# Performance work log

Hardware: AMD Instinct MI355X
Metric: run time of the kernel (lower is better)

## Reference

```python
import jax, jax.numpy as jnp
import numpy as np

SCALE = 1.0
STEPS = 5
ALIGN_CORNERS = True
SHAPE = (2, 3, 128, 128, 128)  # N, C(=3 vector comps), D, H, W


def _identity_grid(spatial, align_corners):
    # spatial = (D, H, W); returns [D, H, W, 3] with coords ordered (x, y, z) in [-1, 1],
    # matching torch.nn.functional.grid_sample's grid convention.
    axes = []
    for s in spatial:
        if align_corners:
            axes.append(jnp.linspace(-1.0, 1.0, s, dtype=jnp.float32))
        else:
            axes.append(((2.0 * jnp.arange(s, dtype=jnp.float32) + 1.0) / s) - 1.0)
    zz, yy, xx = jnp.meshgrid(axes[0], axes[1], axes[2], indexing="ij")  # each [D,H,W]
    return jnp.stack([xx, yy, zz], axis=-1)


def _grid_sample_3d(u, grid, align_corners):
    # u: [N, D, H, W, C] channels-last values; grid: [N, D, H, W, 3] (x, y, z) in [-1, 1].
    # Trilinear interpolation with border padding (deepali expv default: PaddingMode.BORDER).
    N, D, H, W, C = u.shape

    def unnorm(g, size):
        if align_corners:
            return (g + 1.0) * 0.5 * (size - 1)
        return ((g + 1.0) * size - 1.0) * 0.5

    x = jnp.clip(unnorm(grid[..., 0], W), 0.0, W - 1)
    y = jnp.clip(unnorm(grid[..., 1], H), 0.0, H - 1)
    z = jnp.clip(unnorm(grid[..., 2], D), 0.0, D - 1)

    x0f, y0f, z0f = jnp.floor(x), jnp.floor(y), jnp.floor(z)
    wx = (x - x0f)[..., None]  # [N,D,H,W,1]
    wy = (y - y0f)[..., None]
    wz = (z - z0f)[..., None]

    x0 = x0f.astype(jnp.int32); x1 = jnp.minimum(x0 + 1, W - 1)
    y0 = y0f.astype(jnp.int32); y1 = jnp.minimum(y0 + 1, H - 1)
    z0 = z0f.astype(jnp.int32); z1 = jnp.minimum(z0 + 1, D - 1)

    b = jnp.arange(N)[:, None, None, None]  # broadcast batch index [N,1,1,1]

    def gather(zi, yi, xi):
        return u[b, zi, yi, xi]  # [N,D,H,W,C]

    # interpolate along x, then y, then z
    c00 = gather(z0, y0, x0) * (1 - wx) + gather(z0, y0, x1) * wx
    c01 = gather(z0, y1, x0) * (1 - wx) + gather(z0, y1, x1) * wx
    c10 = gather(z1, y0, x0) * (1 - wx) + gather(z1, y0, x1) * wx
    c11 = gather(z1, y1, x0) * (1 - wx) + gather(z1, y1, x1) * wx
    c0 = c00 * (1 - wy) + c01 * wy
    c1 = c10 * (1 - wy) + c11 * wy
    return c0 * (1 - wz) + c1 * wz


def setup_inputs() -> dict:
    key = jax.random.key(0)
    # velocity field: small displacements in normalized cube coordinates
    x = jax.random.normal(key, SHAPE, dtype=jnp.float32) * 0.1
    return {"x": x}


def reference(x) -> jnp.ndarray:
    # expv: scaling-and-squaring exponentiation of velocity field x -> displacement field.
    # u <- scale * x / 2^steps; repeat steps times: u <- u + u o u  (self-composition via warp)
    scale = SCALE / (2 ** STEPS)
    u = jnp.moveaxis(x, 1, -1) * scale  # [N, D, H, W, 3], channels (x, y, z)
    grid0 = _identity_grid(x.shape[2:], ALIGN_CORNERS)  # [D, H, W, 3]
    for _ in range(STEPS):
        u = u + _grid_sample_3d(u, grid0[None] + u, ALIGN_CORNERS)
    return jnp.moveaxis(u, -1, 1)  # back to [N, 3, D, H, W]
```

## Files before the change

kernel.cpp:

```cpp
#include <hip/hip_runtime.h>


namespace {
constexpr int kD = 128, kH = 128, kW = 128, kN = 2, kC = 3;
constexpr int kPlane = kD * kH * kW;
constexpr int kVol   = kC * kPlane;
constexpr int kTotalVox   = kN * kPlane;
constexpr int kTotalElems = kN * kVol;
constexpr size_t kBatchBytes = (size_t)kPlane * 6;
constexpr float kScale0 = 1.0f / 32.0f;
}

typedef float f32x2 __attribute__((ext_vector_type(2)));
typedef unsigned int u32;
typedef u32 u32x3 __attribute__((ext_vector_type(3), aligned(4)));
typedef u32 u32x4a4 __attribute__((ext_vector_type(4), aligned(4)));

static __device__ __forceinline__ float h2f(u32 bits) {
    _Float16 v;
    unsigned short s = (unsigned short)bits;
    __builtin_memcpy(&v, &s, 2);
    return (float)v;
}
static __device__ __forceinline__ u32 f2h2(float a, float b) {
    _Float16 ha = (_Float16)a, hb = (_Float16)b;
    unsigned short sa, sb;
    __builtin_memcpy(&sa, &ha, 2);
    __builtin_memcpy(&sb, &hb, 2);
    return (u32)sa | ((u32)sb << 16);
}

static __device__ __forceinline__ int slab_rr(int* n_out, bool rev) {
    int b    = blockIdx.x;
    int xcd  = b & 7;
    int seq  = b >> 3;
    if (rev) seq = 255 - seq;
    int slab = xcd | (((seq >> 7) & 1) << 3);
    *n_out   = slab >> 3;
    int dblk = slab & 7;
    int s7   = seq & 127;
    int ht   = s7 & 31;
    int dt   = (s7 >> 5) & 3;
    int wl   = threadIdx.x & 63;
    int hh   = (threadIdx.x >> 6) & 3;
    int dd   = (threadIdx.x >> 8) & 3;
    int d    = (dblk << 4) | (dt << 2) | dd;
    int h    = (ht << 2) | hh;
    return (d << 14) | (h << 7) | (wl << 1);
}

__global__ __launch_bounds__(1024) void transcode_kernel(const float* __restrict__ x,
                                                         void* __restrict__ aos) {
    int n;
    int rr = slab_rr(&n, false);
    const float* __restrict__ ub = x + (size_t)n * kVol;
    f32x2 bx = __builtin_nontemporal_load((const f32x2*)(ub + rr));
    f32x2 by = __builtin_nontemporal_load((const f32x2*)(ub + kPlane + rr));
    f32x2 bz = __builtin_nontemporal_load((const f32x2*)(ub + 2 * kPlane + rr));
    bx *= kScale0; by *= kScale0; bz *= kScale0;
    u32x3 s;
    s.x = f2h2(bx.x, by.x);
    s.y = f2h2(bz.x, bz.y);
    s.z = f2h2(bx.y, by.y);
    char* ob = (char*)aos + (size_t)n * kBatchBytes;
    *(u32x3*)(ob + (size_t)(rr >> 1) * 12) = s;
}

template <int MODE, bool REV>
__global__ __launch_bounds__(1024) void step_p6h(const void* __restrict__ uin,
                                                 void* __restrict__ uout) {
    int n;
    int rr = slab_rr(&n, REV);
    int w = rr & 127;
    int h = (rr >> 7) & 127;
    int d = rr >> 14;

    const char* __restrict__ ubase = (const char*)uin + (size_t)n * kBatchBytes;

    u32x3 bq = *(const u32x3*)(ubase + (size_t)(rr >> 1) * 12);
    float vx[2], vy[2], vz[2];
    vx[0] = h2f(bq.x & 0xffffu); vy[0] = h2f(bq.x >> 16); vz[0] = h2f(bq.y & 0xffffu);
    vx[1] = h2f(bq.z & 0xffffu); vy[1] = h2f(bq.z >> 16); vz[1] = h2f(bq.y >> 16);

    int   o[2];
    float wxa[2], wya[2], wza[2];
    #pragma unroll
    for (int j = 0; j < 2; ++j) {
        float px = fminf(fmaxf((float)(w + j) + vx[j] * 63.5f, 0.0f), 127.0f);
        float py = fminf(fmaxf((float)h       + vy[j] * 63.5f, 0.0f), 127.0f);
        float pz = fminf(fmaxf((float)d       + vz[j] * 63.5f, 0.0f), 127.0f);
        int x0 = min((int)floorf(px), 126);
        int y0 = min((int)floorf(py), 126);
        int z0 = min((int)floorf(pz), 126);
        wxa[j] = px - (float)x0;
        wya[j] = py - (float)y0;
        wza[j] = pz - (float)z0;
        o[j] = (z0 << 14) + (y0 << 7) + x0;
    }

    const int rowbyte[4] = {0, 768, 98304, 99072};
    float res[3][2];
    #pragma unroll
    for (int j = 0; j < 2; ++j) {
        float wx = wxa[j], wy = wya[j], wz = wza[j];
        float omx = 1.0f - wx, omy = 1.0f - wy, omz = 1.0f - wz;
        u32 pb = (u32)(o[j] & 1);
        size_t gb = (size_t)(o[j] >> 1) * 12 + (pb << 2);
        float cr[4][3];
        #pragma unroll
        for (int r = 0; r < 4; ++r) {
            u32x4a4 q = *(const u32x4a4*)(ubase + gb + rowbyte[r]);
            u32 xy0 = pb ? q.y : q.x;
            u32 z0b = pb ? (q.x >> 16) : (q.y & 0xffffu);
            u32 xy1 = q.z;
            u32 z1b = pb ? (q.w & 0xffffu) : (q.y >> 16);
            float ax = h2f(xy0 & 0xffffu), ay = h2f(xy0 >> 16), az = h2f(z0b);
            float bx = h2f(xy1 & 0xffffu), by = h2f(xy1 >> 16), bz = h2f(z1b);
            cr[r][0] = ax * omx + bx * wx;
            cr[r][1] = ay * omx + by * wx;
            cr[r][2] = az * omx + bz * wx;
        }
        #pragma unroll
        for (int c = 0; c < 3; ++c) {
            float c0 = cr[0][c] * omy + cr[1][c] * wy;
            float c1 = cr[2][c] * omy + cr[3][c] * wy;
            float base = (c == 0) ? vx[j] : (c == 1) ? vy[j] : vz[j];
            res[c][j] = base + (c0 * omz + c1 * wz);
        }
    }

    if constexpr (MODE == 2) {
        float* __restrict__ obp = (float*)uout + (size_t)n * kVol;
        __builtin_nontemporal_store(f32x2{res[0][0], res[0][1]}, (f32x2*)(obp + rr));
        __builtin_nontemporal_store(f32x2{res[1][0], res[1][1]}, (f32x2*)(obp + kPlane + rr));
        __builtin_nontemporal_store(f32x2{res[2][0], res[2][1]}, (f32x2*)(obp + 2 * kPlane + rr));
    } else {
        u32x3 s;
        s.x = f2h2(res[0][0], res[1][0]);
        s.y = f2h2(res[2][0], res[2][1]);
        s.z = f2h2(res[0][1], res[1][1]);
        char* ob = (char*)uout + (size_t)n * kBatchBytes;
        *(u32x3*)(ob + (size_t)(rr >> 1) * 12) = s;
    }
}

template <bool SCALED>
__global__ __launch_bounds__(256) void step_kernel(const float* __restrict__ u,
                                                   float* __restrict__ out) {
    int b    = blockIdx.x;
    int xcd  = b & 7;
    int seq  = b >> 3;
    int slab = xcd | ((seq >> 9) << 3);
    int n    = slab >> 3;
    int dblk = slab & 7;
    int vo   = ((seq & 511) << 9) | (threadIdx.x << 1);
    int rr   = (dblk << 18) | vo;

    int w = rr & 127;
    int h = (rr >> 7) & 127;
    int d = rr >> 14;

    const float* __restrict__ ub = u + (size_t)n * kVol;

    f32x2 bx = *(const f32x2*)(ub + rr);
    f32x2 by = *(const f32x2*)(ub + kPlane + rr);
    f32x2 bz = *(const f32x2*)(ub + 2 * kPlane + rr);
    if (SCALED) { bx *= kScale0; by *= kScale0; bz *= kScale0; }

    int   o[2];
    float wxa[2], wya[2], wza[2];
    #pragma unroll
    for (int j = 0; j < 2; ++j) {
        float vx = (j == 0) ? bx.x : bx.y;
        float vy = (j == 0) ? by.x : by.y;
        float vz = (j == 0) ? bz.x : bz.y;
        float px = fminf(fmaxf((float)(w + j) + vx * 63.5f, 0.0f), 127.0f);
        float py = fminf(fmaxf((float)h       + vy * 63.5f, 0.0f), 127.0f);
        float pz = fminf(fmaxf((float)d       + vz * 63.5f, 0.0f), 127.0f);
        int x0 = min((int)floorf(px), 126);
        int y0 = min((int)floorf(py), 126);
        int z0 = min((int)floorf(pz), 126);
        wxa[j] = px - (float)x0;
        wya[j] = py - (float)y0;
        wza[j] = pz - (float)z0;
        o[j] = (z0 << 14) + (y0 << 7) + x0;
    }

    const int rowoff[4] = {0, 128, 16384, 16512};
    float res[3][2];
    #pragma unroll
    for (int j = 0; j < 2; ++j) {
        float wx = wxa[j], wy = wya[j], wz = wza[j];
        float omx = 1.0f - wx, omy = 1.0f - wy, omz = 1.0f - wz;
        #pragma unroll
        for (int c = 0; c < 3; ++c) {
            const float* __restrict__ up = ub + c * kPlane;
            f32x2 v00 = *(const f32x2*)(up + o[j] + rowoff[0]);
            f32x2 v01 = *(const f32x2*)(up + o[j] + rowoff[1]);
            f32x2 v10 = *(const f32x2*)(up + o[j] + rowoff[2]);
            f32x2 v11 = *(const f32x2*)(up + o[j] + rowoff[3]);
            if (SCALED) { v00 *= kScale0; v01 *= kScale0; v10 *= kScale0; v11 *= kScale0; }
            float c00 = v00.x * omx + v00.y * wx;
            float c01 = v01.x * omx + v01.y * wx;
            float c10 = v10.x * omx + v10.y * wx;
            float c11 = v11.x * omx + v11.y * wx;
            float c0 = c00 * omy + c01 * wy;
            float c1 = c10 * omy + c11 * wy;
            float s  = c0 * omz + c1 * wz;
            float base = (c == 0) ? ((j == 0) ? bx.x : bx.y)
                       : (c == 1) ? ((j == 0) ? by.x : by.y)
                                  : ((j == 0) ? bz.x : bz.y);
            res[c][j] = base + s;
        }
    }

    float* __restrict__ ob = out + (size_t)n * kVol;
    *(f32x2*)(ob + rr)              = f32x2{res[0][0], res[0][1]};
    *(f32x2*)(ob + kPlane + rr)     = f32x2{res[1][0], res[1][1]};
    *(f32x2*)(ob + 2 * kPlane + rr) = f32x2{res[2][0], res[2][1]};
}

extern "C" void kernel_launch(void* const* d_in, const int* in_sizes, int n_in,
                              void* d_out, int out_size, void* d_ws, size_t ws_size,
                              hipStream_t stream) {
    const float* x = (const float*)d_in[0];
    float* out = (float*)d_out;

    const int grd = kTotalVox / (1024 * 2);
    const size_t need_p6 = (size_t)2 * kN * kBatchBytes + 4096;

    if (ws_size >= need_p6) {
        char* A = (char*)d_ws;
        char* B = A + (size_t)kN * kBatchBytes;
        transcode_kernel<<<grd, 1024, 0, stream>>>(x, A);
        step_p6h<1, true ><<<grd, 1024, 0, stream>>>(A, B);
        step_p6h<1, false><<<grd, 1024, 0, stream>>>(B, A);
        step_p6h<1, true ><<<grd, 1024, 0, stream>>>(A, B);
        step_p6h<1, false><<<grd, 1024, 0, stream>>>(B, A);
        step_p6h<2, true ><<<grd, 1024, 0, stream>>>(A, out);
    } else {
        float* ws = (float*)d_ws;
        const int g256 = kTotalVox / (256 * 2);
        step_kernel<true ><<<g256, 256, 0, stream>>>(x,   out);
        step_kernel<false><<<g256, 256, 0, stream>>>(out, ws);
        step_kernel<false><<<g256, 256, 0, stream>>>(ws,  out);
        step_kernel<false><<<g256, 256, 0, stream>>>(out, ws);
        step_kernel<false><<<g256, 256, 0, stream>>>(ws,  out);
    }
}
```

Measured before the change: 202.5 us.

## Stage neighbor halo tile in LDS for the first three composition steps

Adds a step kernel that cooperatively loads a 9x9 row halo (depth x height, full width) of the packed fp16 field into shared memory, then serves trilinear gathers from LDS when the sample falls inside the tile, falling back to global loads otherwise. It targets the repeated global gathers of the early, small-displacement steps, where samples stay near the voxel. In exchange it adds about 62KB of LDS per 1024-thread block, a barrier, and extra load traffic for halo rows. A duplicate decode_pair call in the LDS path is dead code the compiler should remove.

```diff
diff --git a/kernel.cpp b/kernel.cpp
--- a/kernel.cpp
+++ b/kernel.cpp
@@ -28,6 +28,15 @@
     __builtin_memcpy(&sa, &ha, 2);
     __builtin_memcpy(&sb, &hb, 2);
     return (u32)sa | ((u32)sb << 16);
+}
+static __device__ __forceinline__ void decode_pair(u32 q0, u32 q1, u32 q2, u32 q3,
+                                                   u32 pb, float* a, float* bb) {
+    u32 xy0 = pb ? q1 : q0;
+    u32 z0b = pb ? (q0 >> 16) : (q1 & 0xffffu);
+    u32 xy1 = q2;
+    u32 z1b = pb ? (q3 & 0xffffu) : (q1 >> 16);
+    a[0] = h2f(xy0 & 0xffffu); a[1] = h2f(xy0 >> 16); a[2] = h2f(z0b);
+    bb[0] = h2f(xy1 & 0xffffu); bb[1] = h2f(xy1 >> 16); bb[2] = h2f(z1b);
 }
 
 static __device__ __forceinline__ int slab_rr(int* n_out, bool rev) {
@@ -66,6 +75,130 @@
     *(u32x3*)(ob + (size_t)(rr >> 1) * 12) = s;
 }
 
+template <bool REV>
+__global__ __launch_bounds__(1024) void step_lds(const void* __restrict__ uin,
+                                                 void* __restrict__ uout) {
+    __shared__ u32 sm[81 * 192 + 4];
+
+    int b    = blockIdx.x;
+    int xcd  = b & 7;
+    int seq  = b >> 3;
+    if (REV) seq = 255 - seq;
+    int slab = xcd | (((seq >> 7) & 1) << 3);
+    int n    = slab >> 3;
+    int dblk = slab & 7;
+    int s7   = seq & 127;
+    int ht   = s7 & 31;
+    int dt   = (s7 >> 5) & 3;
+    int h0   = ht << 2;
+    int d0   = (dblk << 4) | (dt << 2);
+
+    const char* __restrict__ ubase = (const char*)uin + (size_t)n * kBatchBytes;
+
+    int hs = h0 - 2, dsb = d0 - 2;
+    for (int idx = threadIdx.x; idx < 81 * 48; idx += 1024) {
+        int row = idx / 48;
+        int c   = idx - row * 48;
+        int id  = row / 9;
+        int ih  = row - id * 9;
+        int gy  = min(max(hs + ih, 0), 127);
+        int gz  = min(max(dsb + id, 0), 127);
+        size_t sb = (size_t)(((gz << 13) | (gy << 6)) * 12) + (size_t)c * 16;
+        u32x4a4 q = *(const u32x4a4*)(ubase + sb);
+        int dw = row * 192 + c * 4;
+        sm[dw] = q.x; sm[dw + 1] = q.y; sm[dw + 2] = q.z; sm[dw + 3] = q.w;
+    }
+    __syncthreads();
+
+    int wl = threadIdx.x & 63;
+    int hh = (threadIdx.x >> 6) & 3;
+    int dd = (threadIdx.x >> 8) & 3;
+    int d  = d0 | dd;
+    int h  = h0 | hh;
+    int w  = wl << 1;
+    int rr = (d << 14) | (h << 7) | w;
+
+    {
+    }
+    int rown = (dd + 2) * 9 + (hh + 2);
+    int dwb  = rown * 192 + wl * 3;
+    u32 b0 = sm[dwb], b1 = sm[dwb + 1], b2 = sm[dwb + 2];
+    float vx[2], vy[2], vz[2];
+    vx[0] = h2f(b0 & 0xffffu); vy[0] = h2f(b0 >> 16); vz[0] = h2f(b1 & 0xffffu);
+    vx[1] = h2f(b2 & 0xffffu); vy[1] = h2f(b2 >> 16); vz[1] = h2f(b1 >> 16);
+
+    int   x0a[2], y0a[2], z0a[2];
+    float wxa[2], wya[2], wza[2];
+    #pragma unroll
+    for (int j = 0; j < 2; ++j) {
+        float px = fminf(fmaxf((float)(w + j) + vx[j] * 63.5f, 0.0f), 127.0f);
+        float py = fminf(fmaxf((float)h       + vy[j] * 63.5f, 0.0f), 127.0f);
+        float pz = fminf(fmaxf((float)d       + vz[j] * 63.5f, 0.0f), 127.0f);
+        int x0 = min((int)floorf(px), 126);
+        int y0 = min((int)floorf(py), 126);
+        int z0 = min((int)floorf(pz), 126);
+        wxa[j] = px - (float)x0;
+        wya[j] = py - (float)y0;
+        wza[j] = pz - (float)z0;
+        x0a[j] = x0; y0a[j] = y0; z0a[j] = z0;
+    }
+
+    const int rowbyte[4] = {0, 768, 98304, 99072};
+    float res[3][2];
+    #pragma unroll
+    for (int j = 0; j < 2; ++j) {
+        float wx = wxa[j], wy = wya[j], wz = wza[j];
+        float omx = 1.0f - wx, omy = 1.0f - wy, omz = 1.0f - wz;
+        int x0 = x0a[j], y0 = y0a[j], z0 = z0a[j];
+        u32 pb = (u32)(x0 & 1);
+        int xp = x0 >> 1;
+        float cr[4][3];
+        unsigned ih = (unsigned)(y0 - h0 + 2);
+        unsigned id = (unsigned)(z0 - d0 + 2);
+        if (ih < 8u && id < 8u) {
+            int r00 = ((int)id * 9 + (int)ih) * 192 + xp * 3 + (int)pb;
+            const int roff[4] = {0, 192, 9 * 192, 10 * 192};
+            #pragma unroll
+            for (int r = 0; r < 4; ++r) {
+                int dw = r00 + roff[r];
+                decode_pair(sm[dw], sm[dw + 1], sm[dw + 2], sm[dw + 3], pb,
+                            cr[r], cr[r]);
+                float a[3], bv[3];
+                decode_pair(sm[dw], sm[dw + 1], sm[dw + 2], sm[dw + 3], pb, a, bv);
+                cr[r][0] = a[0] * omx + bv[0] * wx;
+                cr[r][1] = a[1] * omx + bv[1] * wx;
+                cr[r][2] = a[2] * omx + bv[2] * wx;
+            }
+        } else {
+            int o = (z0 << 14) + (y0 << 7) + x0;
+            size_t gb = (size_t)(o >> 1) * 12 + (pb << 2);
+            #pragma unroll
+            for (int r = 0; r < 4; ++r) {
+                u32x4a4 q = *(const u32x4a4*)(ubase + gb + rowbyte[r]);
+                float a[3], bv[3];
+                decode_pair(q.x, q.y, q.z, q.w, pb, a, bv);
+                cr[r][0] = a[0] * omx + bv[0] * wx;
+                cr[r][1] = a[1] * omx + bv[1] * wx;
+                cr[r][2] = a[2] * omx + bv[2] * wx;
+            }
+        }
+        #pragma unroll
+        for (int c = 0; c < 3; ++c) {
+            float c0 = cr[0][c] * omy + cr[1][c] * wy;
+            float c1 = cr[2][c] * omy + cr[3][c] * wy;
+            float base = (c == 0) ? vx[j] : (c == 1) ? vy[j] : vz[j];
+            res[c][j] = base + (c0 * omz + c1 * wz);
+        }
+    }
+
+    u32x3 s;
+    s.x = f2h2(res[0][0], res[1][0]);
+    s.y = f2h2(res[2][0], res[2][1]);
+    s.z = f2h2(res[0][1], res[1][1]);
+    char* ob = (char*)uout + (size_t)n * kBatchBytes;
+    *(u32x3*)(ob + (size_t)(rr >> 1) * 12) = s;
+}
+
 template <int MODE, bool REV>
 __global__ __launch_bounds__(1024) void step_p6h(const void* __restrict__ uin,
                                                  void* __restrict__ uout) {
@@ -110,15 +243,11 @@
         #pragma unroll
         for (int r = 0; r < 4; ++r) {
             u32x4a4 q = *(const u32x4a4*)(ubase + gb + rowbyte[r]);
-            u32 xy0 = pb ? q.y : q.x;
-            u32 z0b = pb ? (q.x >> 16) : (q.y & 0xffffu);
-            u32 xy1 = q.z;
-            u32 z1b = pb ? (q.w & 0xffffu) : (q.y >> 16);
-            float ax = h2f(xy0 & 0xffffu), ay = h2f(xy0 >> 16), az = h2f(z0b);
-            float bx = h2f(xy1 & 0xffffu), by = h2f(xy1 >> 16), bz = h2f(z1b);
-            cr[r][0] = ax * omx + bx * wx;
-            cr[r][1] = ay * omx + by * wx;
-            cr[r][2] = az * omx + bz * wx;
+            float a[3], bv[3];
+            decode_pair(q.x, q.y, q.z, q.w, pb, a, bv);
+            cr[r][0] = a[0] * omx + bv[0] * wx;
+            cr[r][1] = a[1] * omx + bv[1] * wx;
+            cr[r][2] = a[2] * omx + bv[2] * wx;
         }
         #pragma unroll
         for (int c = 0; c < 3; ++c) {
@@ -233,9 +362,9 @@
         char* A = (char*)d_ws;
         char* B = A + (size_t)kN * kBatchBytes;
         transcode_kernel<<<grd, 1024, 0, stream>>>(x, A);
-        step_p6h<1, true ><<<grd, 1024, 0, stream>>>(A, B);
-        step_p6h<1, false><<<grd, 1024, 0, stream>>>(B, A);
-        step_p6h<1, true ><<<grd, 1024, 0, stream>>>(A, B);
+        step_lds<true ><<<grd, 1024, 0, stream>>>(A, B);
+        step_lds<false><<<grd, 1024, 0, stream>>>(B, A);
+        step_lds<true ><<<grd, 1024, 0, stream>>>(A, B);
         step_p6h<1, false><<<grd, 1024, 0, stream>>>(B, A);
         step_p6h<2, true ><<<grd, 1024, 0, stream>>>(A, out);
     } else {
```

Result: slower. 213.6 us (+5.5%).
